# Kernel optimization log

Measured on AMD Instinct MI355X. Metric: run time of the kernel, lower is better.

The kernel has to match this reference:

```python
import jax, jax.numpy as jnp
import numpy as np

NEG_INF = -1e30  # safe stand-in for float('-inf') under softmax


def setup_inputs() -> dict:
    key = jax.random.key(0)
    ks = jax.random.split(key, 5)
    B, T, D = 4, 2048, 1024
    s = 1.0 / np.sqrt(D)
    return {
        "x": jax.random.normal(ks[0], (B, T, D), dtype=jnp.float32),
        "Wk": jax.random.normal(ks[1], (D, D), dtype=jnp.float32) * s,
        "bk": jnp.zeros((D,), dtype=jnp.float32),
        "Wq": jax.random.normal(ks[2], (D, D), dtype=jnp.float32) * s,
        "bq": jnp.zeros((D,), dtype=jnp.float32),
        "Wv": jax.random.normal(ks[3], (D, D), dtype=jnp.float32) * s,
        "bv": jnp.zeros((D,), dtype=jnp.float32),
        "Wp": jax.random.normal(ks[4], (D, D), dtype=jnp.float32) * s,
        "bp": jnp.zeros((D,), dtype=jnp.float32),
    }


def reference(x, Wk, bk, Wq, bq, Wv, bv, Wp, bp):
    B, T, D = x.shape
    nh = 16
    hd = D // nh
    # QKV projections (weights stored as [in, out])
    q = (x @ Wq + bq).reshape(B, T, nh, hd)
    k = (x @ Wk + bk).reshape(B, T, nh, hd)
    v = (x @ Wv + bv).reshape(B, T, nh, hd)
    # raw attention scores [B, nh, T, T] (module applies no 1/sqrt(d) scale)
    scores = jnp.einsum("bthc,bshc->bhts", q, k)
    causal = jnp.triu(jnp.ones((T, T), dtype=bool), k=1)  # mask future positions
    scores = jnp.where(causal, NEG_INF, scores)
    attn = jax.nn.softmax(scores, axis=-1)  # dropout p=0.0 -> identity
    out = jnp.einsum("bhts,bshc->bthc", attn, v).reshape(B, T, D)
    return out @ Wp + bp
```

## Files before the change

### kernel.cpp

```cpp
#include <hip/hip_runtime.h>
#include <hip/hip_bf16.h>
#include <stdint.h>

#define B_ 4
#define T_ 2048
#define D_ 1024
#define M_ (B_*T_)
#define NH_ 16
#define HD_ 64

typedef __attribute__((ext_vector_type(8))) short bf16x8;
typedef __attribute__((ext_vector_type(4))) float f32x4;

#define GLOAD_LDS16(gp, lp)                                                   \
  __builtin_amdgcn_global_load_lds(                                           \
      (const __attribute__((address_space(1))) void*)(gp),                    \
      (__attribute__((address_space(3))) void*)(lp), 16, 0, 0)

__device__ __forceinline__ unsigned short f2bf(float f) {
  union { float f; unsigned u; } x; x.f = f;
  unsigned r = x.u + 0x7FFFu + ((x.u >> 16) & 1u);
  return (unsigned short)(r >> 16);
}

__global__ __launch_bounds__(256) void cvt_x_kernel(const float* __restrict__ x,
                                                    unsigned short* __restrict__ xb) {
  int i = (blockIdx.x * 256 + threadIdx.x) * 8;
  float4 a = *(const float4*)(x + i);
  float4 b = *(const float4*)(x + i + 4);
  ushort4 lo, hi;
  lo.x = f2bf(a.x); lo.y = f2bf(a.y); lo.z = f2bf(a.z); lo.w = f2bf(a.w);
  hi.x = f2bf(b.x); hi.y = f2bf(b.y); hi.z = f2bf(b.z); hi.w = f2bf(b.w);
  *(ushort4*)(xb + i) = lo;
  *(ushort4*)(xb + i + 4) = hi;
}

__global__ __launch_bounds__(256) void transpose_w4_kernel(
    const float* __restrict__ W0, const float* __restrict__ W1,
    const float* __restrict__ W2, const float* __restrict__ W3,
    unsigned short* __restrict__ O0, unsigned short* __restrict__ O1,
    unsigned short* __restrict__ O2, unsigned short* __restrict__ O3) {
  const float* W = (blockIdx.y == 0) ? W0 : (blockIdx.y == 1) ? W1 : (blockIdx.y == 2) ? W2 : W3;
  unsigned short* Wt = (blockIdx.y == 0) ? O0 : (blockIdx.y == 1) ? O1 : (blockIdx.y == 2) ? O2 : O3;
  __shared__ unsigned short tile[64][72];
  const int bk = (blockIdx.x & 15) * 64;
  const int bn = (blockIdx.x >> 4) * 64;
  const int t = threadIdx.x;
  const int r0 = t >> 4;
  const int c0 = (t & 15) * 4;
#pragma unroll
  for (int p = 0; p < 4; ++p) {
    int r = p * 16 + r0;
    float4 v = *(const float4*)&W[(size_t)(bk + r) * D_ + bn + c0];
    tile[r][c0 + 0] = f2bf(v.x);
    tile[r][c0 + 1] = f2bf(v.y);
    tile[r][c0 + 2] = f2bf(v.z);
    tile[r][c0 + 3] = f2bf(v.w);
  }
  __syncthreads();
#pragma unroll
  for (int p = 0; p < 4; ++p) {
    int n = p * 16 + r0;
    ushort4 o;
    o.x = tile[c0 + 0][n];
    o.y = tile[c0 + 1][n];
    o.z = tile[c0 + 2][n];
    o.w = tile[c0 + 3][n];
    *(ushort4*)&Wt[(size_t)(bn + n) * D_ + bk + c0] = o;
  }
}

__global__ __launch_bounds__(256) void transpose_v_kernel(
    const unsigned short* __restrict__ Vb, unsigned short* __restrict__ Vtg) {
  __shared__ unsigned short tile[64][72];
  const int ct = blockIdx.x * 64;
  const int tt = blockIdx.y * 64;
  const size_t bofs_in  = (size_t)blockIdx.z * T_ * D_;
  const size_t bofs_out = (size_t)blockIdx.z * D_ * T_;
  const int t = threadIdx.x;
  const int r0 = t >> 4;
  const int c0 = (t & 15) * 4;
#pragma unroll
  for (int p = 0; p < 4; ++p) {
    int r = p * 16 + r0;
    *(ushort4*)&tile[r][c0] = *(const ushort4*)&Vb[bofs_in + (size_t)(tt + r) * D_ + ct + c0];
  }
  __syncthreads();
#pragma unroll
  for (int p = 0; p < 4; ++p) {
    int n = p * 16 + r0;
    ushort4 o;
    o.x = tile[c0 + 0][n];
    o.y = tile[c0 + 1][n];
    o.z = tile[c0 + 2][n];
    o.w = tile[c0 + 3][n];
    *(ushort4*)&Vtg[bofs_out + (size_t)(ct + n) * T_ + tt + c0] = o;
  }
}

#define BM 128
#define BN 128
#define BK 64
template <typename OutT>
__device__ __forceinline__ void gemm_core(
    const unsigned short* __restrict__ A, const unsigned short* __restrict__ Bt,
    const float* __restrict__ bias, OutT* __restrict__ C,
    unsigned short* As, unsigned short* Bs, int bm, int bn) {
  const int K = D_, N = D_;
  const int t = threadIdx.x;
  const int lane = t & 63;
  const int w = t >> 6;
  const int wr = (w >> 1) * 64;
  const int wc = (w & 1) * 64;
  const int lr = lane & 15;
  const int lk = (lane >> 4) * 8;
  const int cr = (lane >> 4) * 4;
  const int cc = lane & 15;
  const int srow = lane >> 3;
  const int scol = (lane & 7) * 8;

  f32x4 acc[4][4] = {};

  for (int k0 = 0; k0 < K; k0 += BK) {
#pragma unroll
    for (int i = 0; i < 4; ++i) {
      const int rbase = w * 32 + i * 8;
      GLOAD_LDS16(&A[(size_t)(bm + rbase + srow) * K + k0 + scol], &As[rbase * BK]);
      GLOAD_LDS16(&Bt[(size_t)(bn + rbase + srow) * K + k0 + scol], &Bs[rbase * BK]);
    }
    __syncthreads();
#pragma unroll
    for (int kk = 0; kk < BK; kk += 32) {
      bf16x8 a[4], b[4];
#pragma unroll
      for (int m = 0; m < 4; ++m) a[m] = *(const bf16x8*)&As[(wr + m * 16 + lr) * BK + kk + lk];
#pragma unroll
      for (int n = 0; n < 4; ++n) b[n] = *(const bf16x8*)&Bs[(wc + n * 16 + lr) * BK + kk + lk];
#pragma unroll
      for (int m = 0; m < 4; ++m)
#pragma unroll
        for (int n = 0; n < 4; ++n)
          acc[m][n] = __builtin_amdgcn_mfma_f32_16x16x32_bf16(a[m], b[n], acc[m][n], 0, 0, 0);
    }
    __syncthreads();
  }

#pragma unroll
  for (int m = 0; m < 4; ++m)
#pragma unroll
    for (int n = 0; n < 4; ++n) {
      int col = bn + wc + n * 16 + cc;
      float bv = bias[col];
#pragma unroll
      for (int j = 0; j < 4; ++j) {
        int row = bm + wr + m * 16 + cr + j;
        float v = acc[m][n][j] + bv;
        if constexpr (__is_same(OutT, float)) {
          C[(size_t)row * N + col] = v;
        } else {
          C[(size_t)row * N + col] = f2bf(v);
        }
      }
    }
}

__global__ __launch_bounds__(256) void gemm_qkv_kernel(
    const unsigned short* __restrict__ xb,
    const unsigned short* __restrict__ WqT, const unsigned short* __restrict__ WkT,
    const unsigned short* __restrict__ WvT,
    const float* __restrict__ bq, const float* __restrict__ bk, const float* __restrict__ bv,
    unsigned short* __restrict__ Qb, unsigned short* __restrict__ Kb,
    unsigned short* __restrict__ Vb) {
  __shared__ unsigned short As[BM * BK];
  __shared__ unsigned short Bs[BN * BK];
  const int z = blockIdx.z;
  const unsigned short* Bt = (z == 0) ? WqT : (z == 1) ? WkT : WvT;
  const float* bias = (z == 0) ? bq : (z == 1) ? bk : bv;
  unsigned short* C = (z == 0) ? Qb : (z == 1) ? Kb : Vb;
  const int by = blockIdx.x * 8 + (blockIdx.y & 7);
  const int bx = blockIdx.y >> 3;
  gemm_core<unsigned short>(xb, Bt, bias, C, As, Bs, by * BM, bx * BN);
}

__global__ __launch_bounds__(256) void gemm_proj_kernel(
    const unsigned short* __restrict__ A, const unsigned short* __restrict__ Bt,
    const float* __restrict__ bias, float* __restrict__ C) {
  __shared__ unsigned short As[BM * BK];
  __shared__ unsigned short Bs[BN * BK];
  const int by = blockIdx.x * 8 + (blockIdx.y & 7);
  const int bx = blockIdx.y >> 3;
  gemm_core<float>(A, Bt, bias, C, As, Bs, by * BM, bx * BN);
}

__global__ __launch_bounds__(512, 4) void attn_kernel(
    const unsigned short* __restrict__ Qb,
    const unsigned short* __restrict__ Kb,
    const unsigned short* __restrict__ Vtg,
    unsigned short* __restrict__ Ob)
{
  __shared__ unsigned short Ks[64][72];
  __shared__ unsigned short Vt[64][72];
  __shared__ unsigned int   Ps32[8][16][36];

  const int pid = blockIdx.x;
  const int bh  = blockIdx.y;
  const int b = bh >> 4, h = bh & 15;
  const int t = threadIdx.x;
  const int lane = t & 63;
  const int w = t >> 6;
  const int lr = lane & 15;
  const int g = lane >> 4;
  const int lk = g * 8;
  const int cr = g * 4;
  const int cc = lane & 15;

  const size_t base  = (size_t)(b * T_) * D_ + h * HD_;
  const size_t vbase = ((size_t)b * D_ + h * HD_) * T_;

  const int sr  = t >> 3;
  const int scc = (t & 7) * 8;

  int4 kreg = *(const int4*)&Kb[base + (size_t)sr * D_ + scc];
  int4 vreg = *(const int4*)&Vtg[vbase + (size_t)sr * T_ + scc];

  for (int hp = 0; hp < 2; ++hp) {
    const int qt = (hp == 0) ? pid : 15 - pid;
    const int qtile = qt * 128;
    const int qrow0 = qtile + w * 16;
    const int niter = 2 * qt + 2;

    bf16x8 qf[2];
#pragma unroll
    for (int kk = 0; kk < 2; ++kk)
      qf[kk] = *(const bf16x8*)&Qb[base + (size_t)(qrow0 + lr) * D_ + kk * 32 + lk];

    f32x4 acc_o[4] = {};
    float mrun = -1e30f, lrun = 0.f;

    for (int it = 0; it < niter; ++it) {
      const int kvb = it * 64;
      __syncthreads();
      *(int4*)&Ks[sr][scc] = kreg;
      *(int4*)&Vt[sr][scc] = vreg;
      __syncthreads();
      {
        int nkvb = (it + 1 < niter) ? (it + 1) * 64 : ((hp == 0) ? 0 : -1);
        if (nkvb >= 0) {
          kreg = *(const int4*)&Kb[base + (size_t)(nkvb + sr) * D_ + scc];
          vreg = *(const int4*)&Vtg[vbase + (size_t)sr * T_ + nkvb + scc];
        }
      }

      if (kvb <= qrow0 + 15) {
        f32x4 s[4] = {};
#pragma unroll
        for (int kk = 0; kk < 2; ++kk) {
          bf16x8 kf[4];
#pragma unroll
          for (int n = 0; n < 4; ++n) kf[n] = *(const bf16x8*)&Ks[n * 16 + lr][kk * 32 + lk];
#pragma unroll
          for (int n = 0; n < 4; ++n)
            s[n] = __builtin_amdgcn_mfma_f32_16x16x32_bf16(kf[n], qf[kk], s[n], 0, 0, 0);
        }

        const int qi = qrow0 + lr;
        if (kvb + 63 > qrow0) {
#pragma unroll
          for (int n = 0; n < 4; ++n)
#pragma unroll
            for (int j = 0; j < 4; ++j) {
              int ki = kvb + n * 16 + cr + j;
              if (ki > qi) s[n][j] = -1e30f;
            }
        }

        float tmax = -1e30f;
#pragma unroll
        for (int n = 0; n < 4; ++n)
          tmax = fmaxf(tmax, fmaxf(fmaxf(s[n][0], s[n][1]), fmaxf(s[n][2], s[n][3])));
        tmax = fmaxf(tmax, __shfl_xor(tmax, 16));
        tmax = fmaxf(tmax, __shfl_xor(tmax, 32));

        float sc = 1.f;
        if (!__all(tmax <= mrun + 8.f)) {
          float mnew = fmaxf(mrun, tmax);
          sc = __expf(mrun - mnew);
          mrun = mnew;
#pragma unroll
          for (int j = 0; j < 4; ++j) {
            float scj = __shfl(sc, (lane & 48) | (cr + j));
#pragma unroll
            for (int n = 0; n < 4; ++n) acc_o[n][j] *= scj;
          }
        }

        float psum = 0.f;
#pragma unroll
        for (int n = 0; n < 4; ++n)
#pragma unroll
          for (int j = 0; j < 4; ++j) {
            float p = __expf(s[n][j] - mrun);
            s[n][j] = p;
            psum += p;
          }
        psum += __shfl_xor(psum, 16);
        psum += __shfl_xor(psum, 32);
        lrun = lrun * sc + psum;

#pragma unroll
        for (int n = 0; n < 4; ++n)
#pragma unroll
          for (int hh = 0; hh < 2; ++hh) {
            float lo = s[n][2 * hh], hi = s[n][2 * hh + 1];
            unsigned pk;
            asm("v_cvt_pk_bf16_f32 %0, %1, %2" : "=v"(pk) : "v"(lo), "v"(hi));
            Ps32[w][lr][n * 8 + g * 2 + hh] = pk;
          }

#pragma unroll
        for (int kk = 0; kk < 2; ++kk) {
          bf16x8 pa = *(const bf16x8*)((const unsigned short*)&Ps32[w][lr][0] + kk * 32 + lk);
#pragma unroll
          for (int n = 0; n < 4; ++n) {
            bf16x8 vf = *(const bf16x8*)&Vt[n * 16 + lr][kk * 32 + lk];
            acc_o[n] = __builtin_amdgcn_mfma_f32_16x16x32_bf16(pa, vf, acc_o[n], 0, 0, 0);
          }
        }
      }
    }

#pragma unroll
    for (int j = 0; j < 4; ++j) {
      float inv = 1.0f / __shfl(lrun, (lane & 48) | (cr + j));
#pragma unroll
      for (int n = 0; n < 4; ++n)
        Ob[base + (size_t)(qrow0 + cr + j) * D_ + n * 16 + cc] = f2bf(acc_o[n][j] * inv);
    }
  }
}

extern "C" void kernel_launch(void* const* d_in, const int* in_sizes, int n_in,
                              void* d_out, int out_size, void* d_ws, size_t ws_size,
                              hipStream_t stream) {
  const float* x  = (const float*)d_in[0];
  const float* Wk = (const float*)d_in[1];
  const float* bk = (const float*)d_in[2];
  const float* Wq = (const float*)d_in[3];
  const float* bq = (const float*)d_in[4];
  const float* Wv = (const float*)d_in[5];
  const float* bv = (const float*)d_in[6];
  const float* Wp = (const float*)d_in[7];
  const float* bp = (const float*)d_in[8];

  char* ws = (char*)d_ws;
  unsigned short* xb  = (unsigned short*)(ws);
  unsigned short* Ob  = (unsigned short*)(ws);
  unsigned short* WqT = (unsigned short*)(ws + (16ull << 20));
  unsigned short* WkT = (unsigned short*)(ws + (18ull << 20));
  unsigned short* WvT = (unsigned short*)(ws + (20ull << 20));
  unsigned short* WpT = (unsigned short*)(ws + (22ull << 20));
  unsigned short* Qb  = (unsigned short*)(ws + (24ull << 20));
  unsigned short* Kb  = (unsigned short*)(ws + (40ull << 20));
  unsigned short* Vb  = (unsigned short*)(ws + (56ull << 20));
  unsigned short* Vtg = (unsigned short*)(ws + (72ull << 20));

  hipLaunchKernelGGL(cvt_x_kernel, dim3((M_ * D_) / (256 * 8)), dim3(256), 0, stream, x, xb);
  hipLaunchKernelGGL(transpose_w4_kernel, dim3(256, 4), dim3(256), 0, stream,
                     Wq, Wk, Wv, Wp, WqT, WkT, WvT, WpT);

  hipLaunchKernelGGL(gemm_qkv_kernel, dim3(D_ / BN, M_ / BM, 3), dim3(256), 0, stream,
                     xb, WqT, WkT, WvT, bq, bk, bv, Qb, Kb, Vb);

  hipLaunchKernelGGL(transpose_v_kernel, dim3(16, 32, 4), dim3(256), 0, stream, Vb, Vtg);

  hipLaunchKernelGGL(attn_kernel, dim3(8, 64), dim3(512), 0, stream, Qb, Kb, Vtg, Ob);

  hipLaunchKernelGGL(gemm_proj_kernel, dim3(D_ / BN, M_ / BM), dim3(256), 0, stream,
                     Ob, WpT, bp, (float*)d_out);
}
```

Baseline: 293.2 us.

## Use 128-wide KV tiles in attention and exp2 with log2e folded into Q

Each attention iteration now processes a 128-key tile instead of 64, halving the iteration count and the barriers per query tile. On the diagonal tile it skips score blocks that are fully masked. The Q projection output is pre-scaled by log2(e) so softmax can call the hardware v_exp_f32 (exp2) directly, and the rescale threshold is adjusted to match. LDS usage grows and occupancy hint drops from 4 to 2 blocks per CU, and more registers are needed for the 8 score fragments.

Measured after the change: 300.2 us. 1.02x slower.

```diff
diff --git a/kernel.cpp b/kernel.cpp
--- a/kernel.cpp
+++ b/kernel.cpp
@@ -8,6 +8,7 @@
 #define M_ (B_*T_)
 #define NH_ 16
 #define HD_ 64
+#define LOG2E 1.4426950408889634f
 
 typedef __attribute__((ext_vector_type(8))) short bf16x8;
 typedef __attribute__((ext_vector_type(4))) float f32x4;
@@ -21,6 +22,12 @@
   union { float f; unsigned u; } x; x.f = f;
   unsigned r = x.u + 0x7FFFu + ((x.u >> 16) & 1u);
   return (unsigned short)(r >> 16);
+}
+
+__device__ __forceinline__ float exp2_hw(float x) {
+  float r;
+  asm("v_exp_f32 %0, %1" : "=v"(r) : "v"(x));
+  return r;
 }
 
 __global__ __launch_bounds__(256) void cvt_x_kernel(const float* __restrict__ x,
@@ -105,7 +112,7 @@
 __device__ __forceinline__ void gemm_core(
     const unsigned short* __restrict__ A, const unsigned short* __restrict__ Bt,
     const float* __restrict__ bias, OutT* __restrict__ C,
-    unsigned short* As, unsigned short* Bs, int bm, int bn) {
+    unsigned short* As, unsigned short* Bs, int bm, int bn, float oscale) {
   const int K = D_, N = D_;
   const int t = threadIdx.x;
   const int lane = t & 63;
@@ -154,7 +161,7 @@
 #pragma unroll
       for (int j = 0; j < 4; ++j) {
         int row = bm + wr + m * 16 + cr + j;
-        float v = acc[m][n][j] + bv;
+        float v = (acc[m][n][j] + bv) * oscale;
         if constexpr (__is_same(OutT, float)) {
           C[(size_t)row * N + col] = v;
         } else {
@@ -177,9 +184,10 @@
   const unsigned short* Bt = (z == 0) ? WqT : (z == 1) ? WkT : WvT;
   const float* bias = (z == 0) ? bq : (z == 1) ? bk : bv;
   unsigned short* C = (z == 0) ? Qb : (z == 1) ? Kb : Vb;
+  const float oscale = (z == 0) ? LOG2E : 1.0f;
   const int by = blockIdx.x * 8 + (blockIdx.y & 7);
   const int bx = blockIdx.y >> 3;
-  gemm_core<unsigned short>(xb, Bt, bias, C, As, Bs, by * BM, bx * BN);
+  gemm_core<unsigned short>(xb, Bt, bias, C, As, Bs, by * BM, bx * BN, oscale);
 }
 
 __global__ __launch_bounds__(256) void gemm_proj_kernel(
@@ -189,18 +197,18 @@
   __shared__ unsigned short Bs[BN * BK];
   const int by = blockIdx.x * 8 + (blockIdx.y & 7);
   const int bx = blockIdx.y >> 3;
-  gemm_core<float>(A, Bt, bias, C, As, Bs, by * BM, bx * BN);
-}
-
-__global__ __launch_bounds__(512, 4) void attn_kernel(
+  gemm_core<float>(A, Bt, bias, C, As, Bs, by * BM, bx * BN, 1.0f);
+}
+
+__global__ __launch_bounds__(512, 2) void attn_kernel(
     const unsigned short* __restrict__ Qb,
     const unsigned short* __restrict__ Kb,
     const unsigned short* __restrict__ Vtg,
     unsigned short* __restrict__ Ob)
 {
-  __shared__ unsigned short Ks[64][72];
-  __shared__ unsigned short Vt[64][72];
-  __shared__ unsigned int   Ps32[8][16][36];
+  __shared__ unsigned short Ks[128][72];
+  __shared__ unsigned short Vt[64][136];
+  __shared__ unsigned int   Ps32[8][16][68];
 
   const int pid = blockIdx.x;
   const int bh  = blockIdx.y;
@@ -217,17 +225,21 @@
   const size_t base  = (size_t)(b * T_) * D_ + h * HD_;
   const size_t vbase = ((size_t)b * D_ + h * HD_) * T_;
 
-  const int sr  = t >> 3;
-  const int scc = (t & 7) * 8;
-
-  int4 kreg = *(const int4*)&Kb[base + (size_t)sr * D_ + scc];
-  int4 vreg = *(const int4*)&Vtg[vbase + (size_t)sr * T_ + scc];
+  const int sk = t >> 2;
+  const int kc = (t & 3) * 16;
+  const int sv = t >> 3;
+  const int tc = (t & 7) * 16;
+
+  int4 kreg0 = *(const int4*)&Kb[base + (size_t)sk * D_ + kc];
+  int4 kreg1 = *(const int4*)&Kb[base + (size_t)sk * D_ + kc + 8];
+  int4 vreg0 = *(const int4*)&Vtg[vbase + (size_t)sv * T_ + tc];
+  int4 vreg1 = *(const int4*)&Vtg[vbase + (size_t)sv * T_ + tc + 8];
 
   for (int hp = 0; hp < 2; ++hp) {
     const int qt = (hp == 0) ? pid : 15 - pid;
     const int qtile = qt * 128;
     const int qrow0 = qtile + w * 16;
-    const int niter = 2 * qt + 2;
+    const int niter = qt + 1;
 
     bf16x8 qf[2];
 #pragma unroll
@@ -238,93 +250,98 @@
     float mrun = -1e30f, lrun = 0.f;
 
     for (int it = 0; it < niter; ++it) {
-      const int kvb = it * 64;
+      const int kvb = it * 128;
+      const bool diag = (it == qt);
       __syncthreads();
-      *(int4*)&Ks[sr][scc] = kreg;
-      *(int4*)&Vt[sr][scc] = vreg;
+      *(int4*)&Ks[sk][kc]     = kreg0;
+      *(int4*)&Ks[sk][kc + 8] = kreg1;
+      *(int4*)&Vt[sv][tc]     = vreg0;
+      *(int4*)&Vt[sv][tc + 8] = vreg1;
       __syncthreads();
       {
-        int nkvb = (it + 1 < niter) ? (it + 1) * 64 : ((hp == 0) ? 0 : -1);
+        int nkvb = (it + 1 < niter) ? (it + 1) * 128 : ((hp == 0) ? 0 : -1);
         if (nkvb >= 0) {
-          kreg = *(const int4*)&Kb[base + (size_t)(nkvb + sr) * D_ + scc];
-          vreg = *(const int4*)&Vtg[vbase + (size_t)sr * T_ + nkvb + scc];
-        }
-      }
-
-      if (kvb <= qrow0 + 15) {
-        f32x4 s[4] = {};
-#pragma unroll
-        for (int kk = 0; kk < 2; ++kk) {
-          bf16x8 kf[4];
-#pragma unroll
-          for (int n = 0; n < 4; ++n) kf[n] = *(const bf16x8*)&Ks[n * 16 + lr][kk * 32 + lk];
-#pragma unroll
-          for (int n = 0; n < 4; ++n)
-            s[n] = __builtin_amdgcn_mfma_f32_16x16x32_bf16(kf[n], qf[kk], s[n], 0, 0, 0);
-        }
-
-        const int qi = qrow0 + lr;
-        if (kvb + 63 > qrow0) {
-#pragma unroll
-          for (int n = 0; n < 4; ++n)
+          kreg0 = *(const int4*)&Kb[base + (size_t)(nkvb + sk) * D_ + kc];
+          kreg1 = *(const int4*)&Kb[base + (size_t)(nkvb + sk) * D_ + kc + 8];
+          vreg0 = *(const int4*)&Vtg[vbase + (size_t)sv * T_ + nkvb + tc];
+          vreg1 = *(const int4*)&Vtg[vbase + (size_t)sv * T_ + nkvb + tc + 8];
+        }
+      }
+
+      const int qi = qrow0 + lr;
+      f32x4 s[8];
+#pragma unroll
+      for (int n = 0; n < 8; ++n) {
+        if (diag && n > w) {
+          s[n] = (f32x4){-1e30f, -1e30f, -1e30f, -1e30f};
+        } else {
+          f32x4 acc_s = {};
+#pragma unroll
+          for (int kk = 0; kk < 2; ++kk) {
+            bf16x8 kf = *(const bf16x8*)&Ks[n * 16 + lr][kk * 32 + lk];
+            acc_s = __builtin_amdgcn_mfma_f32_16x16x32_bf16(kf, qf[kk], acc_s, 0, 0, 0);
+          }
+          if (diag && n == w) {
 #pragma unroll
             for (int j = 0; j < 4; ++j) {
               int ki = kvb + n * 16 + cr + j;
-              if (ki > qi) s[n][j] = -1e30f;
+              if (ki > qi) acc_s[j] = -1e30f;
             }
-        }
-
-        float tmax = -1e30f;
-#pragma unroll
-        for (int n = 0; n < 4; ++n)
-          tmax = fmaxf(tmax, fmaxf(fmaxf(s[n][0], s[n][1]), fmaxf(s[n][2], s[n][3])));
-        tmax = fmaxf(tmax, __shfl_xor(tmax, 16));
-        tmax = fmaxf(tmax, __shfl_xor(tmax, 32));
-
-        float sc = 1.f;
-        if (!__all(tmax <= mrun + 8.f)) {
-          float mnew = fmaxf(mrun, tmax);
-          sc = __expf(mrun - mnew);
-          mrun = mnew;
-#pragma unroll
-          for (int j = 0; j < 4; ++j) {
-            float scj = __shfl(sc, (lane & 48) | (cr + j));
-#pragma unroll
-            for (int n = 0; n < 4; ++n) acc_o[n][j] *= scj;
           }
-        }
-
-        float psum = 0.f;
-#pragma unroll
-        for (int n = 0; n < 4; ++n)
-#pragma unroll
-          for (int j = 0; j < 4; ++j) {
-            float p = __expf(s[n][j] - mrun);
-            s[n][j] = p;
-            psum += p;
-          }
-        psum += __shfl_xor(psum, 16);
-        psum += __shfl_xor(psum, 32);
-        lrun = lrun * sc + psum;
-
-#pragma unroll
-        for (int n = 0; n < 4; ++n)
-#pragma unroll
-          for (int hh = 0; hh < 2; ++hh) {
-            float lo = s[n][2 * hh], hi = s[n][2 * hh + 1];
-            unsigned pk;
-            asm("v_cvt_pk_bf16_f32 %0, %1, %2" : "=v"(pk) : "v"(lo), "v"(hi));
-            Ps32[w][lr][n * 8 + g * 2 + hh] = pk;
-          }
-
-#pragma unroll
-        for (int kk = 0; kk < 2; ++kk) {
-          bf16x8 pa = *(const bf16x8*)((const unsigned short*)&Ps32[w][lr][0] + kk * 32 + lk);
-#pragma unroll
-          for (int n = 0; n < 4; ++n) {
-            bf16x8 vf = *(const bf16x8*)&Vt[n * 16 + lr][kk * 32 + lk];
-            acc_o[n] = __builtin_amdgcn_mfma_f32_16x16x32_bf16(pa, vf, acc_o[n], 0, 0, 0);
-          }
+          s[n] = acc_s;
+        }
+      }
+
+      float tmax = -1e30f;
+#pragma unroll
+      for (int n = 0; n < 8; ++n)
+        tmax = fmaxf(tmax, fmaxf(fmaxf(s[n][0], s[n][1]), fmaxf(s[n][2], s[n][3])));
+      tmax = fmaxf(tmax, __shfl_xor(tmax, 16));
+      tmax = fmaxf(tmax, __shfl_xor(tmax, 32));
+
+      float sc = 1.f;
+      if (!__all(tmax <= mrun + 11.5416f)) {
+        float mnew = fmaxf(mrun, tmax);
+        sc = exp2_hw(mrun - mnew);
+        mrun = mnew;
+#pragma unroll
+        for (int j = 0; j < 4; ++j) {
+          float scj = __shfl(sc, (lane & 48) | (cr + j));
+#pragma unroll
+          for (int n = 0; n < 4; ++n) acc_o[n][j] *= scj;
+        }
+      }
+
+      float psum = 0.f;
+#pragma unroll
+      for (int n = 0; n < 8; ++n)
+#pragma unroll
+        for (int j = 0; j < 4; ++j) {
+          float p = exp2_hw(s[n][j] - mrun);
+          s[n][j] = p;
+          psum += p;
+        }
+      psum += __shfl_xor(psum, 16);
+      psum += __shfl_xor(psum, 32);
+      lrun = lrun * sc + psum;
+
+#pragma unroll
+      for (int n = 0; n < 8; ++n)
+#pragma unroll
+        for (int hh = 0; hh < 2; ++hh) {
+          float lo = s[n][2 * hh], hi = s[n][2 * hh + 1];
+          unsigned pk;
+          asm("v_cvt_pk_bf16_f32 %0, %1, %2" : "=v"(pk) : "v"(lo), "v"(hi));
+          Ps32[w][lr][n * 8 + g * 2 + hh] = pk;
+        }
+
+#pragma unroll
+      for (int ss = 0; ss < 4; ++ss) {
+        bf16x8 pa = *(const bf16x8*)((const unsigned short*)&Ps32[w][lr][0] + ss * 32 + lk);
+#pragma unroll
+        for (int n = 0; n < 4; ++n) {
+          bf16x8 vf = *(const bf16x8*)&Vt[n * 16 + lr][ss * 32 + lk];
+          acc_o[n] = __builtin_amdgcn_mfma_f32_16x16x32_bf16(pa, vf, acc_o[n], 0, 0, 0);
         }
       }
     }
```
